# Kernel tuning notes

Measured on AMD Instinct MI355X. Metric: run time of the kernel, lower is better.

The kernel has to match this reference:

```python
import jax, jax.numpy as jnp
import numpy as np

BITS = 4
VALS_PER_I32 = 32 // BITS  # 8 nibbles per int32
MASK = (1 << BITS) - 1


def setup_inputs() -> dict:
    key = jax.random.key(0)
    k1, k2, k3, k4, k5 = jax.random.split(key, 5)
    B, S, IN, OUT = 4, 2048, 4096, 4096
    x = jax.random.normal(k1, (B, S, IN), dtype=jnp.float32)
    # packed 4-bit weights: IN*BITS/32 int32 rows, packed along infeatures
    qweight = jax.random.randint(k2, (IN * BITS // 32, OUT), 0, 2147483647, dtype=jnp.int32)
    scales = jax.random.uniform(k3, (OUT, 1), dtype=jnp.float32) * 0.01 + 0.001
    zeros = jax.random.uniform(k4, (OUT, 1), dtype=jnp.float32) * 0.05
    bias = jax.random.normal(k5, (OUT,), dtype=jnp.float32) * 0.01
    return {"x": x, "qweight": qweight, "scales": scales, "zeros": zeros, "bias": bias}


def _dequant(qweight, scales, zeros):
    # unpack: each int32 row holds VALS_PER_I32 consecutive infeature values (LSB first)
    shifts = (jnp.arange(VALS_PER_I32, dtype=jnp.int32) * BITS)[None, :, None]  # [1, 8, 1]
    q = (qweight[:, None, :] >> shifts) & MASK            # [in/8, 8, out]
    q = q.reshape(-1, qweight.shape[1]).astype(jnp.float32)  # [in, out]
    # old GPTQ format: W[k, n] = scales[n] * q[k, n] - zeros[n]
    return scales.T * q - zeros.T                          # [in, out]


def reference(x, qweight, scales, zeros, bias):
    outshape = x.shape[:-1] + (qweight.shape[1],)
    xf = x.reshape(-1, x.shape[-1]).astype(jnp.float32)    # [M, in]
    W = _dequant(qweight, scales, zeros)                   # [in, out]
    y = xf @ W + bias.astype(jnp.float32)                  # [M, out]
    return y.astype(x.dtype).reshape(outshape)
```

## Files before the change

### kernel.cpp

```cpp
#include <hip/hip_runtime.h>
#include <hip/hip_bf16.h>
#include <stdint.h>


#define BM 256
#define BN 256
#define BK 32
#define NBUF 4

using f32x4  = __attribute__((ext_vector_type(4))) float;
using bf16x8 = __attribute__((ext_vector_type(8))) __bf16;

typedef const uint32_t __attribute__((address_space(1)))* gas_ptr;
typedef uint32_t __attribute__((address_space(3)))* las_ptr;

__device__ __forceinline__ void gl16(const __bf16* g, __bf16* l) {
    __builtin_amdgcn_global_load_lds((gas_ptr)g, (las_ptr)l, 16, 0, 0);
}

__global__ __launch_bounds__(256) void cvt_x_kernel(
    const float* __restrict__ x, __bf16* __restrict__ xb, size_t n8)
{
    size_t i = (size_t)blockIdx.x * 256 + threadIdx.x;
    if (i >= n8) return;
    const f32x4* p = (const f32x4*)(x + i * 8);
    f32x4 a = p[0], b = p[1];
    bf16x8 v;
    v[0] = (__bf16)a[0]; v[1] = (__bf16)a[1]; v[2] = (__bf16)a[2]; v[3] = (__bf16)a[3];
    v[4] = (__bf16)b[0]; v[5] = (__bf16)b[1]; v[6] = (__bf16)b[2]; v[7] = (__bf16)b[3];
    *(bf16x8*)(xb + i * 8) = v;
}

__global__ __launch_bounds__(256) void dequant_w_kernel(
    const int* __restrict__ qw, const float* __restrict__ scales,
    const float* __restrict__ zeros, __bf16* __restrict__ Wt, int N, int K)
{
    __shared__ __align__(16) __bf16 T[64 * 32 * 8];
    const int tid = threadIdx.x;
    const int nTilesN = N >> 6;
    const int kg0 = (blockIdx.x / nTilesN) << 5;
    const int n0  = (blockIdx.x % nTilesN) << 6;

    #pragma unroll
    for (int it = 0; it < 8; ++it) {
        int idx  = it * 256 + tid;
        int kg_l = idx >> 6, n_l = idx & 63;
        int n = n0 + n_l;
        float s = scales[n], nz = -zeros[n];
        uint32_t w  = (uint32_t)qw[(size_t)(kg0 + kg_l) * N + n];
        uint32_t lo = w & 0x0F0F0F0Fu;
        uint32_t hi = (w >> 4) & 0x0F0F0F0Fu;
        bf16x8 v;
        v[0] = (__bf16)fmaf(s, (float)(lo & 0xFFu),         nz);
        v[1] = (__bf16)fmaf(s, (float)(hi & 0xFFu),         nz);
        v[2] = (__bf16)fmaf(s, (float)((lo >> 8)  & 0xFFu), nz);
        v[3] = (__bf16)fmaf(s, (float)((hi >> 8)  & 0xFFu), nz);
        v[4] = (__bf16)fmaf(s, (float)((lo >> 16) & 0xFFu), nz);
        v[5] = (__bf16)fmaf(s, (float)((hi >> 16) & 0xFFu), nz);
        v[6] = (__bf16)fmaf(s, (float)(lo >> 24),           nz);
        v[7] = (__bf16)fmaf(s, (float)(hi >> 24),           nz);
        int slot = kg_l ^ (n_l & 7);
        *(bf16x8*)&T[(size_t)(n_l * 32 + slot) * 8] = v;
    }
    __syncthreads();
    #pragma unroll
    for (int it = 0; it < 8; ++it) {
        int idx  = it * 256 + tid;
        int n_l  = idx >> 5, kg_l = idx & 31;
        bf16x8 v = *(const bf16x8*)&T[(size_t)(n_l * 32 + (kg_l ^ (n_l & 7))) * 8];
        *(bf16x8*)&Wt[(size_t)(n0 + n_l) * K + (size_t)(kg0 + kg_l) * 8] = v;
    }
}

__global__ __launch_bounds__(512) void qgemm8_kernel(
    const __bf16* __restrict__ A, const __bf16* __restrict__ Bt,
    const float* __restrict__ bias, float* __restrict__ out,
    int M, int N, int K)
{
    __shared__ __align__(16) __bf16 Alds[NBUF * BM * BK];
    __shared__ __align__(16) __bf16 Blds[NBUF * BN * BK];

    const int tid = threadIdx.x;
    const int l   = tid & 63;
    const int w   = tid >> 6;
    const int wm  = w >> 2;
    const int wn  = w & 3;
    const int lr  = l & 15;
    const int lg  = l >> 4;

    int bid = (int)blockIdx.x;
    const int nwg = (int)gridDim.x;
    if ((nwg & 7) == 0) bid = (bid & 7) * (nwg >> 3) + (bid >> 3);

    const int nTilesN = N / BN;
    const int brow = (bid / nTilesN) * BM;
    const int bcol = (bid % nTilesN) * BN;

    const int skb  = (l & 3) ^ ((l >> 3) & 3);
    const int srow = w * 32 + (l >> 2);
    const __bf16* aS0 = A  + (size_t)(brow + srow) * K + skb * 8;
    const __bf16* aS1 = aS0 + (size_t)16 * K;
    const __bf16* bS0 = Bt + (size_t)(bcol + srow) * K + skb * 8;
    const __bf16* bS1 = bS0 + (size_t)16 * K;
    __bf16* aD0 = &Alds[(w * 128) * 8];
    __bf16* aD1 = &Alds[(w * 128 + 64) * 8];
    __bf16* bD0 = &Blds[(w * 128) * 8];
    __bf16* bD1 = &Blds[(w * 128 + 64) * 8];

    #define STAGE_A(tt) { const size_t ko = (size_t)(tt) * BK;            \
        const int sb = ((tt) & 3) * (BM * BK);                            \
        gl16(aS0 + ko, aD0 + sb); gl16(aS1 + ko, aD1 + sb); }
    #define STAGE_B(tt) { const size_t ko = (size_t)(tt) * BK;            \
        const int sb = ((tt) & 3) * (BN * BK);                            \
        gl16(bS0 + ko, bD0 + sb); gl16(bS1 + ko, bD1 + sb); }

    f32x4 acc[8][4];
    #pragma unroll
    for (int i = 0; i < 8; ++i)
        #pragma unroll
        for (int j = 0; j < 4; ++j)
            acc[i][j] = (f32x4){0.f, 0.f, 0.f, 0.f};

    const int NT = K / BK;

    const int rslot = lg ^ ((lr >> 1) & 3);

    STAGE_A(0); STAGE_B(0);
    STAGE_A(1); STAGE_B(1);
    STAGE_A(2); STAGE_B(2);
    asm volatile("s_waitcnt vmcnt(8)" ::: "memory");
    __builtin_amdgcn_s_barrier();

    for (int t = 0; t < NT; ++t) {
        const int bo = (t & 3) * (BM * BK);
        const int abase = bo + (wm * 128 + lr) * BK + rslot * 8;
        const int bbase = bo + (wn * 64  + lr) * BK + rslot * 8;
        const bool pre = (t + 3 < NT);
        bf16x8 af[4], af2[4], bfr[4];

        __builtin_amdgcn_sched_barrier(0);

        #pragma unroll
        for (int mf = 0; mf < 4; ++mf)
            af[mf] = *(const bf16x8*)&Alds[abase + mf * 16 * BK];
        #pragma unroll
        for (int nf = 0; nf < 4; ++nf)
            bfr[nf] = *(const bf16x8*)&Blds[bbase + nf * 16 * BK];
        if (pre) STAGE_A(t + 3);
        __builtin_amdgcn_s_setprio(1);
        #pragma unroll
        for (int mf = 0; mf < 4; ++mf)
            #pragma unroll
            for (int nf = 0; nf < 4; ++nf)
                acc[mf][nf] = __builtin_amdgcn_mfma_f32_16x16x32_bf16(
                    af[mf], bfr[nf], acc[mf][nf], 0, 0, 0);
        __builtin_amdgcn_s_setprio(0);

        #pragma unroll
        for (int mf = 0; mf < 4; ++mf)
            af2[mf] = *(const bf16x8*)&Alds[abase + (mf + 4) * 16 * BK];
        if (pre) STAGE_B(t + 3);
        __builtin_amdgcn_s_setprio(1);
        #pragma unroll
        for (int mf = 0; mf < 4; ++mf)
            #pragma unroll
            for (int nf = 0; nf < 4; ++nf)
                acc[mf + 4][nf] = __builtin_amdgcn_mfma_f32_16x16x32_bf16(
                    af2[mf], bfr[nf], acc[mf + 4][nf], 0, 0, 0);
        __builtin_amdgcn_s_setprio(0);

        if (pre)              { asm volatile("s_waitcnt vmcnt(8)" ::: "memory"); }
        else if (t + 2 < NT)  { asm volatile("s_waitcnt vmcnt(4)" ::: "memory"); }
        else                  { asm volatile("s_waitcnt vmcnt(0)" ::: "memory"); }
        __builtin_amdgcn_sched_barrier(0);
        __builtin_amdgcn_s_barrier();
    }

    #pragma unroll
    for (int nf = 0; nf < 4; ++nf) {
        int col = bcol + wn * 64 + nf * 16 + lr;
        float bv = bias[col];
        #pragma unroll
        for (int mf = 0; mf < 8; ++mf) {
            int row = brow + wm * 128 + mf * 16 + lg * 4;
            #pragma unroll
            for (int i = 0; i < 4; ++i)
                out[(size_t)(row + i) * N + col] = acc[mf][nf][i] + bv;
        }
    }
    #undef STAGE_A
    #undef STAGE_B
}

#define FT_M 128
#define FT_N 128
#define FT_K 64
__global__ __launch_bounds__(256) void qgemm_fused_kernel(
    const float* __restrict__ x, const int* __restrict__ qw,
    const float* __restrict__ scales, const float* __restrict__ zeros,
    const float* __restrict__ bias, float* __restrict__ out,
    int M, int N, int K)
{
    __shared__ __align__(16) __bf16 Alds[FT_M * FT_K];
    __shared__ __align__(16) __bf16 Blds[FT_N * FT_K];

    const int tid  = threadIdx.x;
    const int lane = tid & 63;
    const int wave = tid >> 6;
    const int wm = wave >> 1, wn = wave & 1;
    const int lrow = lane & 15, lkb = lane >> 4;

    const int nTilesN = N / FT_N;
    const int brow = (blockIdx.x / nTilesN) * FT_M;
    const int bcol = (blockIdx.x % nTilesN) * FT_N;

    const int bc  = tid & 127;
    const int qr0 = tid >> 7;
    const float s  = scales[bcol + bc];
    const float nz = -zeros[bcol + bc];

    f32x4 acc[4][4];
    #pragma unroll
    for (int i = 0; i < 4; ++i)
        #pragma unroll
        for (int j = 0; j < 4; ++j)
            acc[i][j] = (f32x4){0.f, 0.f, 0.f, 0.f};

    for (int kt = 0; kt < K; kt += FT_K) {
        #pragma unroll
        for (int i = 0; i < 4; ++i) {
            int g  = tid + i * 256;
            int r  = g >> 3;
            int kbg = g & 7;
            const float* p = x + (size_t)(brow + r) * K + kt + kbg * 8;
            f32x4 f0 = *(const f32x4*)p;
            f32x4 f1 = *(const f32x4*)(p + 4);
            bf16x8 v;
            v[0] = (__bf16)f0[0]; v[1] = (__bf16)f0[1];
            v[2] = (__bf16)f0[2]; v[3] = (__bf16)f0[3];
            v[4] = (__bf16)f1[0]; v[5] = (__bf16)f1[1];
            v[6] = (__bf16)f1[2]; v[7] = (__bf16)f1[3];
            int slot = kbg ^ (r & 7);
            *(bf16x8*)&Alds[r * FT_K + slot * 8] = v;
        }
        #pragma unroll
        for (int i = 0; i < 4; ++i) {
            int qr = qr0 + i * 2;
            uint32_t wv = (uint32_t)qw[(size_t)(kt / 8 + qr) * N + bcol + bc];
            uint32_t lo = wv & 0x0F0F0F0Fu;
            uint32_t hi = (wv >> 4) & 0x0F0F0F0Fu;
            bf16x8 v;
            v[0] = (__bf16)fmaf(s, (float)(lo & 0xFFu),         nz);
            v[1] = (__bf16)fmaf(s, (float)(hi & 0xFFu),         nz);
            v[2] = (__bf16)fmaf(s, (float)((lo >> 8)  & 0xFFu), nz);
            v[3] = (__bf16)fmaf(s, (float)((hi >> 8)  & 0xFFu), nz);
            v[4] = (__bf16)fmaf(s, (float)((lo >> 16) & 0xFFu), nz);
            v[5] = (__bf16)fmaf(s, (float)((hi >> 16) & 0xFFu), nz);
            v[6] = (__bf16)fmaf(s, (float)(lo >> 24),           nz);
            v[7] = (__bf16)fmaf(s, (float)(hi >> 24),           nz);
            int slot = qr ^ (bc & 7);
            *(bf16x8*)&Blds[bc * FT_K + slot * 8] = v;
        }
        __syncthreads();

        #pragma unroll
        for (int ks = 0; ks < 2; ++ks) {
            const int slot = (ks * 4 + lkb) ^ (lrow & 7);
            const int abase = (wm * 64 + lrow) * FT_K + slot * 8;
            const int bbase = (wn * 64 + lrow) * FT_K + slot * 8;
            bf16x8 af[4], bfr[4];
            #pragma unroll
            for (int mf = 0; mf < 4; ++mf)
                af[mf] = *(const bf16x8*)&Alds[abase + mf * 16 * FT_K];
            #pragma unroll
            for (int nf = 0; nf < 4; ++nf)
                bfr[nf] = *(const bf16x8*)&Blds[bbase + nf * 16 * FT_K];
            #pragma unroll
            for (int mf = 0; mf < 4; ++mf)
                #pragma unroll
                for (int nf = 0; nf < 4; ++nf)
                    acc[mf][nf] = __builtin_amdgcn_mfma_f32_16x16x32_bf16(
                        af[mf], bfr[nf], acc[mf][nf], 0, 0, 0);
        }
        __syncthreads();
    }

    #pragma unroll
    for (int nf = 0; nf < 4; ++nf) {
        int col = bcol + wn * 64 + nf * 16 + lrow;
        float bv = bias[col];
        #pragma unroll
        for (int mf = 0; mf < 4; ++mf) {
            int row = brow + wm * 64 + mf * 16 + lkb * 4;
            #pragma unroll
            for (int i = 0; i < 4; ++i)
                out[(size_t)(row + i) * N + col] = acc[mf][nf][i] + bv;
        }
    }
}

extern "C" void kernel_launch(void* const* d_in, const int* in_sizes, int n_in,
                              void* d_out, int out_size, void* d_ws, size_t ws_size,
                              hipStream_t stream) {
    const float* x      = (const float*)d_in[0];
    const int*   qw     = (const int*)d_in[1];
    const float* scales = (const float*)d_in[2];
    const float* zeros  = (const float*)d_in[3];
    const float* bias   = (const float*)d_in[4];
    float* out = (float*)d_out;

    const int N = in_sizes[4];
    const int K = (int)(((long long)in_sizes[1] * 8) / N);
    const int M = in_sizes[0] / K;

    const size_t xb_elems = (size_t)M * K;
    const size_t wt_elems = (size_t)N * K;
    const size_t need = (xb_elems + wt_elems) * sizeof(__bf16);

    const bool shapes_ok = (M % BM == 0) && (N % BN == 0) && (K % 256 == 0) &&
                           (K / BK >= 4);

    if (ws_size >= need && shapes_ok) {
        __bf16* xb = (__bf16*)d_ws;
        __bf16* Wt = xb + xb_elems;

        size_t n8 = xb_elems / 8;
        cvt_x_kernel<<<dim3((unsigned)((n8 + 255) / 256)), 256, 0, stream>>>(x, xb, n8);

        dim3 dq_grid((unsigned)(((K / 8) / 32) * (N / 64)));
        dequant_w_kernel<<<dq_grid, 256, 0, stream>>>(qw, scales, zeros, Wt, N, K);

        dim3 grid((M / BM) * (N / BN));
        qgemm8_kernel<<<grid, 512, 0, stream>>>(xb, Wt, bias, out, M, N, K);
    } else {
        dim3 grid((M / FT_M) * (N / FT_N));
        qgemm_fused_kernel<<<grid, 256, 0, stream>>>(x, qw, scales, zeros, bias, out, M, N, K);
    }
}
```

Before: 300.6 us.

## Switch GEMM main loop to double-buffered BK=64 with half-step prefetch

The bf16 MFMA GEMM used to run a 4-deep ring of BK=32 LDS stages with three tiles prefetched ahead. It now uses two buffers of BK=64, each split into two 32-wide halves, and prefetches the next tile's half while the current half is consumed. Each wave now holds all eight A fragments and streams B fragments two at a time, which aims to cut LDS reads of A per MFMA. The cost is a shallower global-load prefetch distance and higher register pressure from keeping eight A fragments live.

```diff
diff --git a/kernel.cpp b/kernel.cpp
--- a/kernel.cpp
+++ b/kernel.cpp
@@ -5,11 +5,10 @@
 
 #define BM 256
 #define BN 256
-#define BK 32
-#define NBUF 4
-
-using f32x4  = __attribute__((ext_vector_type(4))) float;
-using bf16x8 = __attribute__((ext_vector_type(8))) __bf16;
+#define BK 64
+
+using f32x4   = __attribute__((ext_vector_type(4))) float;
+using bf16x8  = __attribute__((ext_vector_type(8))) __bf16;
 
 typedef const uint32_t __attribute__((address_space(1)))* gas_ptr;
 typedef uint32_t __attribute__((address_space(3)))* las_ptr;
@@ -77,8 +76,8 @@
     const float* __restrict__ bias, float* __restrict__ out,
     int M, int N, int K)
 {
-    __shared__ __align__(16) __bf16 Alds[NBUF * BM * BK];
-    __shared__ __align__(16) __bf16 Blds[NBUF * BN * BK];
+    __shared__ __align__(16) __bf16 Alds[2 * 2 * 256 * 32];
+    __shared__ __align__(16) __bf16 Blds[2 * 2 * 256 * 32];
 
     const int tid = threadIdx.x;
     const int l   = tid & 63;
@@ -98,21 +97,17 @@
 
     const int skb  = (l & 3) ^ ((l >> 3) & 3);
     const int srow = w * 32 + (l >> 2);
-    const __bf16* aS0 = A  + (size_t)(brow + srow) * K + skb * 8;
-    const __bf16* aS1 = aS0 + (size_t)16 * K;
-    const __bf16* bS0 = Bt + (size_t)(bcol + srow) * K + skb * 8;
-    const __bf16* bS1 = bS0 + (size_t)16 * K;
-    __bf16* aD0 = &Alds[(w * 128) * 8];
-    __bf16* aD1 = &Alds[(w * 128 + 64) * 8];
-    __bf16* bD0 = &Blds[(w * 128) * 8];
-    __bf16* bD1 = &Blds[(w * 128 + 64) * 8];
-
-    #define STAGE_A(tt) { const size_t ko = (size_t)(tt) * BK;            \
-        const int sb = ((tt) & 3) * (BM * BK);                            \
-        gl16(aS0 + ko, aD0 + sb); gl16(aS1 + ko, aD1 + sb); }
-    #define STAGE_B(tt) { const size_t ko = (size_t)(tt) * BK;            \
-        const int sb = ((tt) & 3) * (BN * BK);                            \
-        gl16(bS0 + ko, bD0 + sb); gl16(bS1 + ko, bD1 + sb); }
+    const __bf16* aSrc = A  + (size_t)(brow + srow) * K + skb * 8;
+    const __bf16* bSrc = Bt + (size_t)(bcol + srow) * K + skb * 8;
+    __bf16* aDst = &Alds[(size_t)w * 2 * 512];
+    __bf16* bDst = &Blds[(size_t)w * 2 * 512];
+
+    #define STAGE_A(tt, kh) { const size_t ko = (size_t)(tt) * BK + (kh) * 32;  \
+        __bf16* d = aDst + ((((tt) & 1) * 2 + (kh)) * 8192);                    \
+        gl16(aSrc + ko, d); gl16(aSrc + 16 * (size_t)K + ko, d + 512); }
+    #define STAGE_B(tt, kh) { const size_t ko = (size_t)(tt) * BK + (kh) * 32;  \
+        __bf16* d = bDst + ((((tt) & 1) * 2 + (kh)) * 8192);                    \
+        gl16(bSrc + ko, d); gl16(bSrc + 16 * (size_t)K + ko, d + 512); }
 
     f32x4 acc[8][4];
     #pragma unroll
@@ -123,57 +118,76 @@
 
     const int NT = K / BK;
 
-    const int rslot = lg ^ ((lr >> 1) & 3);
-
-    STAGE_A(0); STAGE_B(0);
-    STAGE_A(1); STAGE_B(1);
-    STAGE_A(2); STAGE_B(2);
-    asm volatile("s_waitcnt vmcnt(8)" ::: "memory");
-    __builtin_amdgcn_s_barrier();
+    const int rsp = lg ^ ((lr >> 1) & 3);
+    const int aoff = (wm * 128 + lr) * 32 + rsp * 8;
+    const int boff = (wn * 64  + lr) * 32 + rsp * 8;
+
+    STAGE_A(0, 0); STAGE_B(0, 0);
+    STAGE_A(0, 1); STAGE_B(0, 1);
 
     for (int t = 0; t < NT; ++t) {
-        const int bo = (t & 3) * (BM * BK);
-        const int abase = bo + (wm * 128 + lr) * BK + rslot * 8;
-        const int bbase = bo + (wn * 64  + lr) * BK + rslot * 8;
-        const bool pre = (t + 3 < NT);
-        bf16x8 af[4], af2[4], bfr[4];
-
-        __builtin_amdgcn_sched_barrier(0);
-
-        #pragma unroll
-        for (int mf = 0; mf < 4; ++mf)
-            af[mf] = *(const bf16x8*)&Alds[abase + mf * 16 * BK];
-        #pragma unroll
-        for (int nf = 0; nf < 4; ++nf)
-            bfr[nf] = *(const bf16x8*)&Blds[bbase + nf * 16 * BK];
-        if (pre) STAGE_A(t + 3);
-        __builtin_amdgcn_s_setprio(1);
-        #pragma unroll
-        for (int mf = 0; mf < 4; ++mf)
-            #pragma unroll
-            for (int nf = 0; nf < 4; ++nf)
-                acc[mf][nf] = __builtin_amdgcn_mfma_f32_16x16x32_bf16(
-                    af[mf], bfr[nf], acc[mf][nf], 0, 0, 0);
-        __builtin_amdgcn_s_setprio(0);
-
-        #pragma unroll
-        for (int mf = 0; mf < 4; ++mf)
-            af2[mf] = *(const bf16x8*)&Alds[abase + (mf + 4) * 16 * BK];
-        if (pre) STAGE_B(t + 3);
-        __builtin_amdgcn_s_setprio(1);
-        #pragma unroll
-        for (int mf = 0; mf < 4; ++mf)
-            #pragma unroll
-            for (int nf = 0; nf < 4; ++nf)
-                acc[mf + 4][nf] = __builtin_amdgcn_mfma_f32_16x16x32_bf16(
-                    af2[mf], bfr[nf], acc[mf + 4][nf], 0, 0, 0);
-        __builtin_amdgcn_s_setprio(0);
-
-        if (pre)              { asm volatile("s_waitcnt vmcnt(8)" ::: "memory"); }
-        else if (t + 2 < NT)  { asm volatile("s_waitcnt vmcnt(4)" ::: "memory"); }
-        else                  { asm volatile("s_waitcnt vmcnt(0)" ::: "memory"); }
+        const int bb  = (t & 1) * 16384;
+        const bool pre = (t + 1 < NT);
+        bf16x8 af[8], bf0, bf1;
+
+        asm volatile("s_waitcnt vmcnt(4)" ::: "memory");
         __builtin_amdgcn_sched_barrier(0);
         __builtin_amdgcn_s_barrier();
+        __builtin_amdgcn_sched_barrier(0);
+        #pragma unroll
+        for (int mf = 0; mf < 8; ++mf)
+            af[mf] = *(const bf16x8*)&Alds[bb + aoff + mf * 512];
+        bf0 = *(const bf16x8*)&Blds[bb + boff];
+        bf1 = *(const bf16x8*)&Blds[bb + boff + 512];
+        if (pre) STAGE_A(t + 1, 0);
+        __builtin_amdgcn_s_setprio(1);
+        #pragma unroll
+        for (int mf = 0; mf < 8; ++mf) {
+            acc[mf][0] = __builtin_amdgcn_mfma_f32_16x16x32_bf16(af[mf], bf0, acc[mf][0], 0, 0, 0);
+            acc[mf][1] = __builtin_amdgcn_mfma_f32_16x16x32_bf16(af[mf], bf1, acc[mf][1], 0, 0, 0);
+        }
+        __builtin_amdgcn_s_setprio(0);
+
+        bf0 = *(const bf16x8*)&Blds[bb + boff + 2 * 512];
+        bf1 = *(const bf16x8*)&Blds[bb + boff + 3 * 512];
+        if (pre) STAGE_B(t + 1, 0);
+        __builtin_amdgcn_s_setprio(1);
+        #pragma unroll
+        for (int mf = 0; mf < 8; ++mf) {
+            acc[mf][2] = __builtin_amdgcn_mfma_f32_16x16x32_bf16(af[mf], bf0, acc[mf][2], 0, 0, 0);
+            acc[mf][3] = __builtin_amdgcn_mfma_f32_16x16x32_bf16(af[mf], bf1, acc[mf][3], 0, 0, 0);
+        }
+        __builtin_amdgcn_s_setprio(0);
+
+        if (pre) { asm volatile("s_waitcnt vmcnt(4)" ::: "memory"); }
+        else     { asm volatile("s_waitcnt vmcnt(0)" ::: "memory"); }
+        __builtin_amdgcn_sched_barrier(0);
+        __builtin_amdgcn_s_barrier();
+        __builtin_amdgcn_sched_barrier(0);
+        #pragma unroll
+        for (int mf = 0; mf < 8; ++mf)
+            af[mf] = *(const bf16x8*)&Alds[bb + 8192 + aoff + mf * 512];
+        bf0 = *(const bf16x8*)&Blds[bb + 8192 + boff];
+        bf1 = *(const bf16x8*)&Blds[bb + 8192 + boff + 512];
+        if (pre) STAGE_A(t + 1, 1);
+        __builtin_amdgcn_s_setprio(1);
+        #pragma unroll
+        for (int mf = 0; mf < 8; ++mf) {
+            acc[mf][0] = __builtin_amdgcn_mfma_f32_16x16x32_bf16(af[mf], bf0, acc[mf][0], 0, 0, 0);
+            acc[mf][1] = __builtin_amdgcn_mfma_f32_16x16x32_bf16(af[mf], bf1, acc[mf][1], 0, 0, 0);
+        }
+        __builtin_amdgcn_s_setprio(0);
+
+        bf0 = *(const bf16x8*)&Blds[bb + 8192 + boff + 2 * 512];
+        bf1 = *(const bf16x8*)&Blds[bb + 8192 + boff + 3 * 512];
+        if (pre) STAGE_B(t + 1, 1);
+        __builtin_amdgcn_s_setprio(1);
+        #pragma unroll
+        for (int mf = 0; mf < 8; ++mf) {
+            acc[mf][2] = __builtin_amdgcn_mfma_f32_16x16x32_bf16(af[mf], bf0, acc[mf][2], 0, 0, 0);
+            acc[mf][3] = __builtin_amdgcn_mfma_f32_16x16x32_bf16(af[mf], bf1, acc[mf][3], 0, 0, 0);
+        }
+        __builtin_amdgcn_s_setprio(0);
     }
 
     #pragma unroll
@@ -318,7 +332,7 @@
     const size_t need = (xb_elems + wt_elems) * sizeof(__bf16);
 
     const bool shapes_ok = (M % BM == 0) && (N % BN == 0) && (K % 256 == 0) &&
-                           (K / BK >= 4);
+                           (K / BK >= 2);
 
     if (ws_size >= need && shapes_ok) {
         __bf16* xb = (__bf16*)d_ws;
```

After: 294.8 us (median of 2 runs). No clear change (-1.9%).
